# Kernel tuning notes

Hardware: AMD Instinct MI355X
Metric: run time of the kernel (lower is better)

## Reference

```python
import jax, jax.numpy as jnp
import numpy as np
import math

B, S, H = 4, 1024, 1024
NH, DH = 16, 64  # MULTI_HEAD, HIDDEN_SIZE_HEAD


def setup_inputs() -> dict:
    key = jax.random.key(0)
    ks = jax.random.split(key, 14)
    w = lambda k: (jax.random.normal(k, (H, H), dtype=jnp.float32) * 0.02)
    b = lambda k: (jax.random.normal(k, (H,), dtype=jnp.float32) * 0.02)
    return {
        "v": jax.random.normal(ks[0], (B, S, H), dtype=jnp.float32),
        "k": jax.random.normal(ks[1], (B, S, H), dtype=jnp.float32),
        "q": jax.random.normal(ks[2], (B, S, H), dtype=jnp.float32),
        "mask": jax.random.randint(ks[3], (B, 1, 1, S), 0, 2) == 1,
        "group_prob": jax.random.uniform(ks[4], (B, S, S), dtype=jnp.float32),
        "Wq": w(ks[5]), "bq": b(ks[6]),
        "Wk": w(ks[7]), "bk": b(ks[8]),
        "Wv": w(ks[9]), "bv": b(ks[10]),
        "Wm": w(ks[11]), "bm": b(ks[12]),
    }


def reference(v, k, q, mask, group_prob, Wq, bq, Wk, bk, Wv, bv, Wm, bm):
    nb = q.shape[0]
    inv_sqrt_dk = 1.0 / math.sqrt(DH)

    def proj(x, W, b):
        # torch Linear: x @ W.T + b, then split heads -> [B, NH, S, DH]
        y = jnp.einsum('bsh,oh->bso', x, W) + b
        return y.reshape(nb, -1, NH, DH).transpose(0, 2, 1, 3)

    qh = proj(q, Wq, bq)
    kh = proj(k, Wk, bk)
    vh = proj(v, Wv, bv)

    scores = jnp.einsum('bhqd,bhkd->bhqk', qh, kh) * inv_sqrt_dk
    scores = jnp.where(mask, jnp.float32(-1e9), scores)
    att = jax.nn.softmax(scores, axis=-1)
    # post-softmax group-prior scaling (the non-standard part)
    att = att * group_prob[:, None, :, :]
    # dropout in eval mode = identity
    out = jnp.einsum('bhqk,bhkd->bhqd', att, vh)
    out = out.transpose(0, 2, 1, 3).reshape(nb, -1, H)
    return jnp.einsum('bsh,oh->bso', out, Wm) + bm
```

## Files before the change

### kernel.cpp

```cpp
#include <hip/hip_runtime.h>

#define S_LEN 1024
#define NHEAD 16
#define DHEAD 64

typedef _Float16 half8 __attribute__((ext_vector_type(8)));
typedef _Float16 half4v __attribute__((ext_vector_type(4)));
typedef float floatx4 __attribute__((ext_vector_type(4)));

#define QSCALE 0.125f
#define EXPSHIFT 4.0f

__device__ __forceinline__ void gll16(const _Float16* g, _Float16* s) {
    __builtin_amdgcn_global_load_lds(
        (const __attribute__((address_space(1))) void*)g,
        (__attribute__((address_space(3))) void*)s, 16, 0, 0);
}

struct SplitArgs {
    const float* src[7];
    _Float16* hi[7];
    int nblk[7];
};

__global__ __launch_bounds__(256) void split_all_kernel(SplitArgs a)
{
    int blk = blockIdx.x, seg = 0, off = 0;
    while (blk >= off + a.nblk[seg]) { off += a.nblk[seg]; ++seg; }
    const int base = (blk - off) * 4096 + threadIdx.x * 4;
#pragma unroll
    for (int u = 0; u < 4; ++u) {
        const int i = base + u * 1024;
        float4 v = *(const float4*)&a.src[seg][i];
        half4v h;
        h.x = (_Float16)v.x; h.y = (_Float16)v.y;
        h.z = (_Float16)v.z; h.w = (_Float16)v.w;
        *(half4v*)&a.hi[seg][i] = h;
    }
}

__global__ __launch_bounds__(256) void gp_prep_kernel(
    const float* __restrict__ gp, _Float16* __restrict__ gpt)
{
    __shared__ _Float16 G[128 * 64];
    const int t = threadIdx.x;
    const int tile = blockIdx.x;
    const int kt = tile & 15, qt = (tile >> 4) & 7, b = tile >> 7;
    const float* src = gp + ((size_t)(b * S_LEN + qt * 128)) * S_LEN + kt * 64;

#pragma unroll
    for (int it = 0; it < 8; ++it) {
        const int idx = it * 256 + t;
        const int q = idx >> 4, kk = (idx & 15) * 4;
        float4 v = *(const float4*)&src[(size_t)q * S_LEN + kk];
        half4v h;
        h.x = (_Float16)v.x; h.y = (_Float16)v.y;
        h.z = (_Float16)v.z; h.w = (_Float16)v.w;
        *(half4v*)&G[q * 64 + kk] = h;
    }
    __syncthreads();

    _Float16* dst = gpt + (size_t)tile * 8192;
#pragma unroll
    for (int ph = 0; ph < 4; ++ph) {
        const int chunk = ph * 256 + t;
        const int l = chunk & 63;
        const int rest = chunk >> 6;
        const int h2 = rest & 1, mt = (rest >> 1) & 1, w = rest >> 2;
        const int qb = w * 32 + mt * 16 + (l >> 4) * 4;
        const int kb = l & 15;
        half8 o;
#pragma unroll
        for (int jj = 0; jj < 2; ++jj)
#pragma unroll
            for (int rg = 0; rg < 4; ++rg)
                o[jj * 4 + rg] = G[(qb + rg) * 64 + kb + (h2 * 2 + jj) * 16];
        *(half8*)&dst[chunk * 8] = o;
    }
}

struct ProjArgs {
    const _Float16* A[3];
    const _Float16* B[3];
    const float* bias[3];
    _Float16* C[3];
};

__global__ __launch_bounds__(256, 3) void proj_gemm_kernel(ProjArgs p)
{
    __shared__ __align__(16) _Float16 Ab[128 * 64];
    __shared__ __align__(16) _Float16 Bb[128 * 64];

    const int bid = blockIdx.x;
    const int xcd = bid & 7;
    const int slot = bid >> 3;
    const int mg = slot & 3;
    const int bx = (slot >> 2) & 7;
    const int z  = slot >> 5;
    const int by = xcd + mg * 8;

    const _Float16* A = p.A[z];
    const _Float16* B = p.B[z];
    const float* bias = p.bias[z];
    _Float16* C = p.C[z];

    const int t = threadIdx.x;
    const int w = t >> 6;
    const int l = t & 63;
    const int r = l & 15;
    const int quad = l >> 4;
    const int k7 = r & 7;
    const int rr = l >> 3, ii = l & 7;
    const int wm = (w >> 1) * 64, wn = (w & 1) * 64;
    const int m0 = by * 128;
    const int n0 = bx * 128;

    floatx4 acc[4][4];
#pragma unroll
    for (int i = 0; i < 4; ++i)
#pragma unroll
        for (int j = 0; j < 4; ++j) acc[i][j] = (floatx4){0.f, 0.f, 0.f, 0.f};

    const _Float16* ssrc = (w < 2) ? A : B;
    _Float16* sdst = (w < 2) ? Ab : Bb;
    const int srow0 = (w < 2) ? m0 : n0;
    const int w01 = w & 1;

    auto stage = [&](int kt) {
        const int k0 = kt * 64;
#pragma unroll
        for (int c = 0; c < 8; ++c) {
            const int R = w01 * 64 + c * 8 + rr;
            const int j = ii ^ (R & 7);
            gll16(ssrc + (size_t)(srow0 + R) * 1024 + k0 + j * 8,
                  sdst + R * 64 + ii * 8);
        }
    };

    stage(0);
    for (int kt = 0; kt < 16; ++kt) {
        __syncthreads();

        half8 ah[4][2], bh[4][2];
#pragma unroll
        for (int i = 0; i < 4; ++i) {
            const int R = wm + i * 16 + r;
            ah[i][0] = *(const half8*)&Ab[R * 64 + ((quad ^ k7) << 3)];
            ah[i][1] = *(const half8*)&Ab[R * 64 + (((4 | quad) ^ k7) << 3)];
        }
#pragma unroll
        for (int j = 0; j < 4; ++j) {
            const int R = wn + j * 16 + r;
            bh[j][0] = *(const half8*)&Bb[R * 64 + ((quad ^ k7) << 3)];
            bh[j][1] = *(const half8*)&Bb[R * 64 + (((4 | quad) ^ k7) << 3)];
        }
        __syncthreads();

        if (kt + 1 < 16) stage(kt + 1);

#pragma unroll
        for (int c = 0; c < 2; ++c)
#pragma unroll
            for (int i = 0; i < 4; ++i)
#pragma unroll
                for (int j = 0; j < 4; ++j)
                    acc[i][j] = __builtin_amdgcn_mfma_f32_16x16x32_f16(
                        ah[i][c], bh[j][c], acc[i][j], 0, 0, 0);
    }

#pragma unroll
    for (int i = 0; i < 4; ++i)
#pragma unroll
        for (int j = 0; j < 4; ++j) {
            const int n = n0 + wn + j * 16 + r;
            const float bv = bias[n];
#pragma unroll
            for (int reg = 0; reg < 4; ++reg) {
                const int m = m0 + wm + i * 16 + quad * 4 + reg;
                float val = acc[i][j][reg] + bv;
                if (z == 0) val *= QSCALE;
                const int b = m >> 10, s = m & 1023;
                const int h = n >> 6, d = n & 63;
                const size_t idx = (z == 2)
                    ? (((size_t)(b * NHEAD + h)) * DHEAD + d) * S_LEN + s
                    : (((size_t)(b * NHEAD + h)) * S_LEN + s) * DHEAD + d;
                C[idx] = (_Float16)val;
            }
        }
}

__global__ __launch_bounds__(256, 2) void out_gemm_kernel(
    const _Float16* __restrict__ A, const _Float16* __restrict__ B,
    const float* __restrict__ bias, float* __restrict__ C)
{
    __shared__ __align__(16) _Float16 Ab[128 * 64];
    __shared__ __align__(16) _Float16 Bb[64 * 64];

    const int bid = blockIdx.x;
    const int xcd = bid & 7;
    const int slot = bid >> 3;
    const int by = xcd + (slot & 3) * 8;
    const int bx = slot >> 2;

    const int t = threadIdx.x;
    const int w = t >> 6;
    const int l = t & 63;
    const int r = l & 15;
    const int quad = l >> 4;
    const int k7 = r & 7;
    const int rr = l >> 3, ii = l & 7;
    const int m0 = by * 128, n0 = bx * 64;

    floatx4 acc[2][4];
#pragma unroll
    for (int mt = 0; mt < 2; ++mt)
#pragma unroll
        for (int j = 0; j < 4; ++j) acc[mt][j] = (floatx4){0.f, 0.f, 0.f, 0.f};

    auto stage = [&](int kt) {
        const int k0 = kt * 64;
        if (w < 2) {
#pragma unroll
            for (int c = 0; c < 8; ++c) {
                const int R = (w & 1) * 64 + c * 8 + rr;
                const int j = ii ^ (R & 7);
                gll16(A + (size_t)(m0 + R) * 1024 + k0 + j * 8,
                      Ab + R * 64 + ii * 8);
            }
        } else {
#pragma unroll
            for (int c = 0; c < 4; ++c) {
                const int R = (w - 2) * 32 + c * 8 + rr;
                const int j = ii ^ (R & 7);
                gll16(B + (size_t)(n0 + R) * 1024 + k0 + j * 8,
                      Bb + R * 64 + ii * 8);
            }
        }
    };

    stage(0);
    for (int kt = 0; kt < 16; ++kt) {
        __syncthreads();

        half8 ah[2][2], bh[4][2];
#pragma unroll
        for (int mt = 0; mt < 2; ++mt) {
            const int R = w * 32 + mt * 16 + r;
            ah[mt][0] = *(const half8*)&Ab[R * 64 + ((quad ^ k7) << 3)];
            ah[mt][1] = *(const half8*)&Ab[R * 64 + (((4 | quad) ^ k7) << 3)];
        }
#pragma unroll
        for (int j = 0; j < 4; ++j) {
            const int R = j * 16 + r;
            bh[j][0] = *(const half8*)&Bb[R * 64 + ((quad ^ k7) << 3)];
            bh[j][1] = *(const half8*)&Bb[R * 64 + (((4 | quad) ^ k7) << 3)];
        }
        __syncthreads();

        if (kt + 1 < 16) stage(kt + 1);

#pragma unroll
        for (int c = 0; c < 2; ++c)
#pragma unroll
            for (int mt = 0; mt < 2; ++mt)
#pragma unroll
                for (int j = 0; j < 4; ++j)
                    acc[mt][j] = __builtin_amdgcn_mfma_f32_16x16x32_f16(
                        ah[mt][c], bh[j][c], acc[mt][j], 0, 0, 0);
    }

#pragma unroll
    for (int mt = 0; mt < 2; ++mt)
#pragma unroll
        for (int j = 0; j < 4; ++j) {
            const int n = n0 + j * 16 + r;
            const float bv = bias[n];
#pragma unroll
            for (int reg = 0; reg < 4; ++reg) {
                const int m = m0 + w * 32 + mt * 16 + quad * 4 + reg;
                C[(size_t)m * 1024 + n] = acc[mt][j][reg] + bv;
            }
        }
}

__global__ __launch_bounds__(256, 4) void attention_mfma_kernel(
    const _Float16* __restrict__ Qhi, const _Float16* __restrict__ Khi,
    const _Float16* __restrict__ Vthi, const _Float16* __restrict__ gpt,
    const int* __restrict__ mask, _Float16* __restrict__ OutHi)
{
    __shared__ __align__(16) _Float16 KhS[2][4096];
    __shared__ __align__(16) _Float16 VhS[2][4096];
    __shared__ __align__(16) _Float16 PS[4096];

    const int t = threadIdx.x;
    const int w = t >> 6;
    const int l = t & 63;
    const int lr = l & 15;
    const int quad = l >> 4;
    const int rr = l >> 3;
    const int ii = l & 7;

    const int h   = blockIdx.x & 15;
    const int qt2 = (blockIdx.x >> 4) & 15;
    const int b   = blockIdx.x >> 8;
    const int q0  = qt2 * 64;
    const size_t hb = (size_t)(b * NHEAD + h) * (S_LEN * DHEAD);
    const _Float16* gptile = gpt + (size_t)((b * 8 + (qt2 >> 1)) * 16) * 8192;
    const int wold = (qt2 & 1) * 2 + (w >> 1);
    const int mtold = w & 1;

    half8 qfh[2];
#pragma unroll
    for (int c = 0; c < 2; ++c) {
        const size_t off = hb + (size_t)(q0 + w * 16 + lr) * 64 + c * 32 + quad * 8;
        qfh[c] = *(const half8*)&Qhi[off];
    }

    float lpart[4];
    floatx4 Oa[4];
#pragma unroll
    for (int rg = 0; rg < 4; ++rg) {
        lpart[rg] = 0.0f;
        Oa[rg] = (floatx4){0.f, 0.f, 0.f, 0.f};
    }

    auto stageK = [&](int kt, int bf) {
        const int k0n = kt * 64;
#pragma unroll
        for (int c2 = 0; c2 < 2; ++c2) {
            const int c = w * 2 + c2;
            const int row = c * 8 + rr;
            const int j = ii ^ (row & 7);
            gll16(Khi + hb + (size_t)(k0n + row) * 64 + j * 8,
                  &KhS[bf][0] + c * 512 + l * 8);
        }
    };
    auto stageV = [&](int kt, int bf) {
        const int k0n = kt * 64;
#pragma unroll
        for (int c2 = 0; c2 < 2; ++c2) {
            const int i = w * 2 + c2;
            const int row = i * 8 + rr;
            const int j = ii ^ (row & 7);
            gll16(Vthi + hb + (size_t)row * S_LEN + k0n + j * 8,
                  &VhS[bf][0] + i * 512 + l * 8);
        }
    };
    auto loadG = [&](half8 (&g)[2], int kt) {
#pragma unroll
        for (int h2 = 0; h2 < 2; ++h2)
            g[h2] = *(const half8*)&gptile[(size_t)kt * 8192 +
                (((wold * 2 + mtold) * 2 + h2) * 64 + l) * 8];
    };

    half8 gc[2], gn[2];
    stageK(0, 0);
    stageV(0, 0);
    loadG(gc, 0);
    __syncthreads();

    for (int kt = 0; kt < 16; ++kt) {
        const int bf = kt & 1;
        const int k0 = kt * 64;

        if (kt + 1 < 16) {
            stageK(kt + 1, bf ^ 1);
            stageV(kt + 1, bf ^ 1);
            loadG(gn, kt + 1);
        }

        int mk[4];
#pragma unroll
        for (int j = 0; j < 4; ++j) mk[j] = mask[b * S_LEN + k0 + j * 16 + lr];

        floatx4 sc[4];
#pragma unroll
        for (int j = 0; j < 4; ++j) sc[j] = (floatx4){0.f, 0.f, 0.f, 0.f};

#pragma unroll
        for (int j = 0; j < 4; ++j) {
            const int key = j * 16 + lr;
            const int base = key * 64;
            const int k7a = key & 7;
            const half8 kh0 = *(const half8*)&KhS[bf][base + (quad ^ k7a) * 8];
            const half8 kh1 = *(const half8*)&KhS[bf][base + ((4 + quad) ^ k7a) * 8];
            floatx4 a = sc[j];
            a = __builtin_amdgcn_mfma_f32_16x16x32_f16(qfh[0], kh0, a, 0, 0, 0);
            a = __builtin_amdgcn_mfma_f32_16x16x32_f16(qfh[1], kh1, a, 0, 0, 0);
            sc[j] = a;
        }

        {
            const int qlb = w * 16 + quad * 4;
#pragma unroll
            for (int j = 0; j < 4; ++j) {
                const int col = j * 16 + lr;
                const int cc = col >> 3, wi = col & 7;
                const half8 g = (j < 2) ? gc[0] : gc[1];
#pragma unroll
                for (int rg = 0; rg < 4; ++rg) {
                    const float e = __expf(sc[j][rg] - EXPSHIFT);
                    const float p = mk[j] ? 0.0f : e;
                    lpart[rg] += p;
                    const _Float16 res = (_Float16)p * g[(j & 1) * 4 + rg];
                    const int qloc = qlb + rg;
                    PS[qloc * 64 + (cc ^ (qloc & 7)) * 8 + wi] = res;
                }
            }
        }

        half8 pf[2];
        {
            const int qloc = w * 16 + lr;
            const int q7 = qloc & 7;
            pf[0] = *(const half8*)&PS[qloc * 64 + (quad ^ q7) * 8];
            pf[1] = *(const half8*)&PS[qloc * 64 + ((4 + quad) ^ q7) * 8];
        }
#pragma unroll
        for (int dt = 0; dt < 4; ++dt) {
            const int d = dt * 16 + lr;
            const int base = d * 64, d7 = d & 7;
            const half8 vh0 = *(const half8*)&VhS[bf][base + (quad ^ d7) * 8];
            const half8 vh1 = *(const half8*)&VhS[bf][base + ((4 + quad) ^ d7) * 8];
            floatx4 a = Oa[dt];
            a = __builtin_amdgcn_mfma_f32_16x16x32_f16(pf[0], vh0, a, 0, 0, 0);
            a = __builtin_amdgcn_mfma_f32_16x16x32_f16(pf[1], vh1, a, 0, 0, 0);
            Oa[dt] = a;
        }

        __syncthreads();

        if (kt + 1 < 16) {
#pragma unroll
            for (int h2 = 0; h2 < 2; ++h2) gc[h2] = gn[h2];
        }
    }

#pragma unroll
    for (int rg = 0; rg < 4; ++rg) {
#pragma unroll
        for (int off = 1; off < 16; off <<= 1)
            lpart[rg] += __shfl_xor(lpart[rg], off, 64);
    }

#pragma unroll
    for (int rg = 0; rg < 4; ++rg) {
        const int s = q0 + w * 16 + quad * 4 + rg;
        const float linv = 1.0f / lpart[rg];
#pragma unroll
        for (int dt = 0; dt < 4; ++dt) {
            const float val = Oa[dt][rg] * linv;
            const size_t idx = ((size_t)(b * S_LEN + s)) * 1024 + h * 64 + dt * 16 + lr;
            OutHi[idx] = (_Float16)val;
        }
    }
}

extern "C" void kernel_launch(void* const* d_in, const int* in_sizes, int n_in,
                              void* d_out, int out_size, void* d_ws, size_t ws_size,
                              hipStream_t stream) {
    const float* v    = (const float*)d_in[0];
    const float* k    = (const float*)d_in[1];
    const float* q    = (const float*)d_in[2];
    const int*   mask = (const int*)d_in[3];
    const float* gp   = (const float*)d_in[4];
    const float* Wq   = (const float*)d_in[5];
    const float* bq   = (const float*)d_in[6];
    const float* Wk   = (const float*)d_in[7];
    const float* bk   = (const float*)d_in[8];
    const float* Wv   = (const float*)d_in[9];
    const float* bv   = (const float*)d_in[10];
    const float* Wm   = (const float*)d_in[11];
    const float* bm   = (const float*)d_in[12];
    float* out = (float*)d_out;

    uint8_t* w8 = (uint8_t*)d_ws;
    const size_t MB = 1024 * 1024;
    _Float16* q_h  = (_Float16*)(w8 + 0 * MB);
    _Float16* k_h  = (_Float16*)(w8 + 8 * MB);
    _Float16* v_h  = (_Float16*)(w8 + 16 * MB);
    _Float16* Wq_h = (_Float16*)(w8 + 24 * MB);
    _Float16* Wk_h = (_Float16*)(w8 + 26 * MB);
    _Float16* Wv_h = (_Float16*)(w8 + 28 * MB);
    _Float16* Wm_h = (_Float16*)(w8 + 30 * MB);
    _Float16* Qh   = (_Float16*)(w8 + 32 * MB);
    _Float16* Kh   = (_Float16*)(w8 + 40 * MB);
    _Float16* Vt   = (_Float16*)(w8 + 48 * MB);
    _Float16* gpt  = (_Float16*)(w8 + 56 * MB);
    _Float16* at   = (_Float16*)(w8 + 0 * MB);

    SplitArgs sa;
    sa.src[0] = q;  sa.hi[0] = q_h;  sa.nblk[0] = 1024;
    sa.src[1] = k;  sa.hi[1] = k_h;  sa.nblk[1] = 1024;
    sa.src[2] = v;  sa.hi[2] = v_h;  sa.nblk[2] = 1024;
    sa.src[3] = Wq; sa.hi[3] = Wq_h; sa.nblk[3] = 256;
    sa.src[4] = Wk; sa.hi[4] = Wk_h; sa.nblk[4] = 256;
    sa.src[5] = Wv; sa.hi[5] = Wv_h; sa.nblk[5] = 256;
    sa.src[6] = Wm; sa.hi[6] = Wm_h; sa.nblk[6] = 256;
    split_all_kernel<<<4096, 256, 0, stream>>>(sa);

    gp_prep_kernel<<<512, 256, 0, stream>>>(gp, gpt);

    ProjArgs pa;
    pa.A[0] = q_h; pa.B[0] = Wq_h; pa.bias[0] = bq; pa.C[0] = Qh;
    pa.A[1] = k_h; pa.B[1] = Wk_h; pa.bias[1] = bk; pa.C[1] = Kh;
    pa.A[2] = v_h; pa.B[2] = Wv_h; pa.bias[2] = bv; pa.C[2] = Vt;
    proj_gemm_kernel<<<768, 256, 0, stream>>>(pa);

    attention_mfma_kernel<<<1024, 256, 0, stream>>>(
        Qh, Kh, Vt, gpt, mask, at);

    out_gemm_kernel<<<512, 256, 0, stream>>>(
        at, Wm_h, bm, out);
}
```

Baseline: 232.3 us.

## Fold mask into additive bias, transpose score MFMA, drop gp prep kernel

Removes the separate group_prob transpose kernel and converts group_prob to plain fp16 inside the shared split kernel, which also precomputes a float additive mask bias. The attention kernel swaps the MFMA operands so each lane holds four consecutive keys for one query row. This lets the mask bias seed the accumulator, lets group_prob be read as contiguous half4 loads, and lets the P tile be written as vectorized half4 stores with a single running row sum. It also remaps block IDs across XCDs. The trade-offs are more scattered global reads of gp rows and a fallback that writes the mask bias into the output buffer when the workspace is too small.

```diff
diff --git a/kernel.cpp b/kernel.cpp
--- a/kernel.cpp
+++ b/kernel.cpp
@@ -6,10 +6,12 @@
 
 typedef _Float16 half8 __attribute__((ext_vector_type(8)));
 typedef _Float16 half4v __attribute__((ext_vector_type(4)));
+typedef _Float16 half2v __attribute__((ext_vector_type(2)));
 typedef float floatx4 __attribute__((ext_vector_type(4)));
 
 #define QSCALE 0.125f
 #define EXPSHIFT 4.0f
+#define MASKBIAS -30000.0f
 
 __device__ __forceinline__ void gll16(const _Float16* g, _Float16* s) {
     __builtin_amdgcn_global_load_lds(
@@ -18,14 +20,29 @@
 }
 
 struct SplitArgs {
-    const float* src[7];
-    _Float16* hi[7];
-    int nblk[7];
+    const float* src[8];
+    _Float16* hi[8];
+    int nblk[8];
+    const int* mask;
+    float* mbias;
 };
 
 __global__ __launch_bounds__(256) void split_all_kernel(SplitArgs a)
 {
-    int blk = blockIdx.x, seg = 0, off = 0;
+    int blk = blockIdx.x;
+    if (blk < 4) {
+        const int i = blk * 1024 + threadIdx.x * 4;
+        int4 m = *(const int4*)&a.mask[i];
+        float4 o;
+        o.x = m.x ? MASKBIAS : 0.0f;
+        o.y = m.y ? MASKBIAS : 0.0f;
+        o.z = m.z ? MASKBIAS : 0.0f;
+        o.w = m.w ? MASKBIAS : 0.0f;
+        *(float4*)&a.mbias[i] = o;
+        return;
+    }
+    blk -= 4;
+    int seg = 0, off = 0;
     while (blk >= off + a.nblk[seg]) { off += a.nblk[seg]; ++seg; }
     const int base = (blk - off) * 4096 + threadIdx.x * 4;
 #pragma unroll
@@ -36,46 +53,6 @@
         h.x = (_Float16)v.x; h.y = (_Float16)v.y;
         h.z = (_Float16)v.z; h.w = (_Float16)v.w;
         *(half4v*)&a.hi[seg][i] = h;
-    }
-}
-
-__global__ __launch_bounds__(256) void gp_prep_kernel(
-    const float* __restrict__ gp, _Float16* __restrict__ gpt)
-{
-    __shared__ _Float16 G[128 * 64];
-    const int t = threadIdx.x;
-    const int tile = blockIdx.x;
-    const int kt = tile & 15, qt = (tile >> 4) & 7, b = tile >> 7;
-    const float* src = gp + ((size_t)(b * S_LEN + qt * 128)) * S_LEN + kt * 64;
-
-#pragma unroll
-    for (int it = 0; it < 8; ++it) {
-        const int idx = it * 256 + t;
-        const int q = idx >> 4, kk = (idx & 15) * 4;
-        float4 v = *(const float4*)&src[(size_t)q * S_LEN + kk];
-        half4v h;
-        h.x = (_Float16)v.x; h.y = (_Float16)v.y;
-        h.z = (_Float16)v.z; h.w = (_Float16)v.w;
-        *(half4v*)&G[q * 64 + kk] = h;
-    }
-    __syncthreads();
-
-    _Float16* dst = gpt + (size_t)tile * 8192;
-#pragma unroll
-    for (int ph = 0; ph < 4; ++ph) {
-        const int chunk = ph * 256 + t;
-        const int l = chunk & 63;
-        const int rest = chunk >> 6;
-        const int h2 = rest & 1, mt = (rest >> 1) & 1, w = rest >> 2;
-        const int qb = w * 32 + mt * 16 + (l >> 4) * 4;
-        const int kb = l & 15;
-        half8 o;
-#pragma unroll
-        for (int jj = 0; jj < 2; ++jj)
-#pragma unroll
-            for (int rg = 0; rg < 4; ++rg)
-                o[jj * 4 + rg] = G[(qb + rg) * 64 + kb + (h2 * 2 + jj) * 16];
-        *(half8*)&dst[chunk * 8] = o;
     }
 }
 
@@ -285,8 +262,8 @@
 
 __global__ __launch_bounds__(256, 4) void attention_mfma_kernel(
     const _Float16* __restrict__ Qhi, const _Float16* __restrict__ Khi,
-    const _Float16* __restrict__ Vthi, const _Float16* __restrict__ gpt,
-    const int* __restrict__ mask, _Float16* __restrict__ OutHi)
+    const _Float16* __restrict__ Vthi, const _Float16* __restrict__ gp16,
+    const float* __restrict__ mbias, _Float16* __restrict__ OutHi)
 {
     __shared__ __align__(16) _Float16 KhS[2][4096];
     __shared__ __align__(16) _Float16 VhS[2][4096];
@@ -300,29 +277,27 @@
     const int rr = l >> 3;
     const int ii = l & 7;
 
-    const int h   = blockIdx.x & 15;
-    const int qt2 = (blockIdx.x >> 4) & 15;
-    const int b   = blockIdx.x >> 8;
+    const int Lid = ((blockIdx.x & 7) << 7) | (blockIdx.x >> 3);
+    const int h   = Lid & 15;
+    const int qt2 = (Lid >> 4) & 15;
+    const int b   = Lid >> 8;
     const int q0  = qt2 * 64;
     const size_t hb = (size_t)(b * NHEAD + h) * (S_LEN * DHEAD);
-    const _Float16* gptile = gpt + (size_t)((b * 8 + (qt2 >> 1)) * 16) * 8192;
-    const int wold = (qt2 & 1) * 2 + (w >> 1);
-    const int mtold = w & 1;
+    const int qg = q0 + w * 16 + lr;
+    const _Float16* gprow = gp16 + ((size_t)(b * S_LEN + qg)) * S_LEN;
+    const float* mb = mbias + b * S_LEN;
 
     half8 qfh[2];
 #pragma unroll
     for (int c = 0; c < 2; ++c) {
-        const size_t off = hb + (size_t)(q0 + w * 16 + lr) * 64 + c * 32 + quad * 8;
+        const size_t off = hb + (size_t)qg * 64 + c * 32 + quad * 8;
         qfh[c] = *(const half8*)&Qhi[off];
     }
 
-    float lpart[4];
+    float lpart = 0.0f;
     floatx4 Oa[4];
 #pragma unroll
-    for (int rg = 0; rg < 4; ++rg) {
-        lpart[rg] = 0.0f;
-        Oa[rg] = (floatx4){0.f, 0.f, 0.f, 0.f};
-    }
+    for (int dt = 0; dt < 4; ++dt) Oa[dt] = (floatx4){0.f, 0.f, 0.f, 0.f};
 
     auto stageK = [&](int kt, int bf) {
         const int k0n = kt * 64;
@@ -346,37 +321,36 @@
                   &VhS[bf][0] + i * 512 + l * 8);
         }
     };
-    auto loadG = [&](half8 (&g)[2], int kt) {
-#pragma unroll
-        for (int h2 = 0; h2 < 2; ++h2)
-            g[h2] = *(const half8*)&gptile[(size_t)kt * 8192 +
-                (((wold * 2 + mtold) * 2 + h2) * 64 + l) * 8];
+    auto loadGM = [&](half4v (&g)[4], floatx4 (&m)[4], int kt) {
+        const int k0n = kt * 64;
+#pragma unroll
+        for (int j = 0; j < 4; ++j) {
+            const int kk = k0n + j * 16 + quad * 4;
+            g[j] = *(const half4v*)&gprow[kk];
+            m[j] = *(const floatx4*)&mb[kk];
+        }
     };
 
-    half8 gc[2], gn[2];
+    half4v g4c[4], g4n[4];
+    floatx4 mbc[4], mbn[4];
     stageK(0, 0);
     stageV(0, 0);
-    loadG(gc, 0);
+    loadGM(g4c, mbc, 0);
     __syncthreads();
+
+    const int qloc = w * 16 + lr;
+    const int q7 = qloc & 7;
 
     for (int kt = 0; kt < 16; ++kt) {
         const int bf = kt & 1;
-        const int k0 = kt * 64;
 
         if (kt + 1 < 16) {
             stageK(kt + 1, bf ^ 1);
             stageV(kt + 1, bf ^ 1);
-            loadG(gn, kt + 1);
-        }
-
-        int mk[4];
-#pragma unroll
-        for (int j = 0; j < 4; ++j) mk[j] = mask[b * S_LEN + k0 + j * 16 + lr];
+            loadGM(g4n, mbn, kt + 1);
+        }
 
         floatx4 sc[4];
-#pragma unroll
-        for (int j = 0; j < 4; ++j) sc[j] = (floatx4){0.f, 0.f, 0.f, 0.f};
-
 #pragma unroll
         for (int j = 0; j < 4; ++j) {
             const int key = j * 16 + lr;
@@ -384,38 +358,34 @@
             const int k7a = key & 7;
             const half8 kh0 = *(const half8*)&KhS[bf][base + (quad ^ k7a) * 8];
             const half8 kh1 = *(const half8*)&KhS[bf][base + ((4 + quad) ^ k7a) * 8];
-            floatx4 a = sc[j];
-            a = __builtin_amdgcn_mfma_f32_16x16x32_f16(qfh[0], kh0, a, 0, 0, 0);
-            a = __builtin_amdgcn_mfma_f32_16x16x32_f16(qfh[1], kh1, a, 0, 0, 0);
+            floatx4 a = mbc[j];
+            a = __builtin_amdgcn_mfma_f32_16x16x32_f16(kh0, qfh[0], a, 0, 0, 0);
+            a = __builtin_amdgcn_mfma_f32_16x16x32_f16(kh1, qfh[1], a, 0, 0, 0);
             sc[j] = a;
         }
 
-        {
-            const int qlb = w * 16 + quad * 4;
-#pragma unroll
-            for (int j = 0; j < 4; ++j) {
-                const int col = j * 16 + lr;
-                const int cc = col >> 3, wi = col & 7;
-                const half8 g = (j < 2) ? gc[0] : gc[1];
-#pragma unroll
-                for (int rg = 0; rg < 4; ++rg) {
-                    const float e = __expf(sc[j][rg] - EXPSHIFT);
-                    const float p = mk[j] ? 0.0f : e;
-                    lpart[rg] += p;
-                    const _Float16 res = (_Float16)p * g[(j & 1) * 4 + rg];
-                    const int qloc = qlb + rg;
-                    PS[qloc * 64 + (cc ^ (qloc & 7)) * 8 + wi] = res;
-                }
-            }
+#pragma unroll
+        for (int j = 0; j < 4; ++j) {
+            const float p0 = __expf(sc[j][0] - EXPSHIFT);
+            const float p1 = __expf(sc[j][1] - EXPSHIFT);
+            const float p2 = __expf(sc[j][2] - EXPSHIFT);
+            const float p3 = __expf(sc[j][3] - EXPSHIFT);
+            lpart += (p0 + p1) + (p2 + p3);
+            half2v a01 = {(_Float16)p0, (_Float16)p1};
+            half2v a23 = {(_Float16)p2, (_Float16)p3};
+            const half2v g01 = {g4c[j].x, g4c[j].y};
+            const half2v g23 = {g4c[j].z, g4c[j].w};
+            a01 *= g01;
+            a23 *= g23;
+            half4v res;
+            res.x = a01.x; res.y = a01.y; res.z = a23.x; res.w = a23.y;
+            const int ch = j * 2 + (quad >> 1);
+            *(half4v*)&PS[qloc * 64 + ((ch ^ q7) << 3) + (quad & 1) * 4] = res;
         }
 
         half8 pf[2];
-        {
-            const int qloc = w * 16 + lr;
-            const int q7 = qloc & 7;
-            pf[0] = *(const half8*)&PS[qloc * 64 + (quad ^ q7) * 8];
-            pf[1] = *(const half8*)&PS[qloc * 64 + ((4 + quad) ^ q7) * 8];
-        }
+        pf[0] = *(const half8*)&PS[qloc * 64 + ((quad ^ q7) << 3)];
+        pf[1] = *(const half8*)&PS[qloc * 64 + (((4 + quad) ^ q7) << 3)];
 #pragma unroll
         for (int dt = 0; dt < 4; ++dt) {
             const int d = dt * 16 + lr;
@@ -432,24 +402,20 @@
 
         if (kt + 1 < 16) {
 #pragma unroll
-            for (int h2 = 0; h2 < 2; ++h2) gc[h2] = gn[h2];
-        }
-    }
+            for (int j = 0; j < 4; ++j) { g4c[j] = g4n[j]; mbc[j] = mbn[j]; }
+        }
+    }
+
+    lpart += __shfl_xor(lpart, 16, 64);
+    lpart += __shfl_xor(lpart, 32, 64);
 
 #pragma unroll
     for (int rg = 0; rg < 4; ++rg) {
-#pragma unroll
-        for (int off = 1; off < 16; off <<= 1)
-            lpart[rg] += __shfl_xor(lpart[rg], off, 64);
-    }
-
-#pragma unroll
-    for (int rg = 0; rg < 4; ++rg) {
+        const float li = 1.0f / __shfl(lpart, quad * 4 + rg, 64);
         const int s = q0 + w * 16 + quad * 4 + rg;
-        const float linv = 1.0f / lpart[rg];
 #pragma unroll
         for (int dt = 0; dt < 4; ++dt) {
-            const float val = Oa[dt][rg] * linv;
+            const float val = Oa[dt][rg] * li;
             const size_t idx = ((size_t)(b * S_LEN + s)) * 1024 + h * 64 + dt * 16 + lr;
             OutHi[idx] = (_Float16)val;
         }
@@ -486,8 +452,10 @@
     _Float16* Qh   = (_Float16*)(w8 + 32 * MB);
     _Float16* Kh   = (_Float16*)(w8 + 40 * MB);
     _Float16* Vt   = (_Float16*)(w8 + 48 * MB);
-    _Float16* gpt  = (_Float16*)(w8 + 56 * MB);
+    _Float16* gp16 = (_Float16*)(w8 + 56 * MB);
     _Float16* at   = (_Float16*)(w8 + 0 * MB);
+    float* mb_f = (ws_size >= 64 * MB + 16384)
+                ? (float*)(w8 + 64 * MB) : (float*)d_out;
 
     SplitArgs sa;
     sa.src[0] = q;  sa.hi[0] = q_h;  sa.nblk[0] = 1024;
@@ -497,9 +465,10 @@
     sa.src[4] = Wk; sa.hi[4] = Wk_h; sa.nblk[4] = 256;
     sa.src[5] = Wv; sa.hi[5] = Wv_h; sa.nblk[5] = 256;
     sa.src[6] = Wm; sa.hi[6] = Wm_h; sa.nblk[6] = 256;
-    split_all_kernel<<<4096, 256, 0, stream>>>(sa);
-
-    gp_prep_kernel<<<512, 256, 0, stream>>>(gp, gpt);
+    sa.src[7] = gp; sa.hi[7] = gp16; sa.nblk[7] = 1024;
+    sa.mask = mask;
+    sa.mbias = mb_f;
+    split_all_kernel<<<5124, 256, 0, stream>>>(sa);
 
     ProjArgs pa;
     pa.A[0] = q_h; pa.B[0] = Wq_h; pa.bias[0] = bq; pa.C[0] = Qh;
@@ -508,7 +477,7 @@
     proj_gemm_kernel<<<768, 256, 0, stream>>>(pa);
 
     attention_mfma_kernel<<<1024, 256, 0, stream>>>(
-        Qh, Kh, Vt, gpt, mask, at);
+        Qh, Kh, Vt, gp16, mb_f, at);
 
     out_gemm_kernel<<<512, 256, 0, stream>>>(
         at, Wm_h, bm, out);
```

New measurement: 248.0 us. +6.8%, slower.
